# Performance work log

Measured on AMD Instinct MI355X. Metric: run time of the kernel, lower is better.

The kernel has to match this reference:

```python
import jax, jax.numpy as jnp
import numpy as np

B, T, L, H = 16, 16, 512, 768


def setup_inputs() -> dict:
    key = jax.random.key(0)
    k1, k2, k3, k4, k5, k6 = jax.random.split(key, 6)
    hn = jax.random.normal(k1, (B, L, H), dtype=jnp.float32)
    decoder_out = jax.random.normal(k2, (B, L, H), dtype=jnp.float32)
    W1 = jax.random.normal(k3, (H, H), dtype=jnp.float32) * (1.0 / np.sqrt(H))
    W2 = jax.random.normal(k4, (H, H), dtype=jnp.float32) * (1.0 / np.sqrt(H))
    V = jax.random.normal(k5, (H,), dtype=jnp.float32) * (1.0 / np.sqrt(H))
    # Ragged, consistent pointer indices: T monotone segment starts per sample,
    # gold boundary Yindex[b,t] in [Xindex[b,t], L).
    step = L // T  # 32
    Xindex = jnp.broadcast_to(jnp.arange(T, dtype=jnp.int64) * step, (B, T))
    offsets = jax.random.randint(k6, (B, T), 0, step, dtype=jnp.int64)
    Yindex = Xindex + offsets
    lens = jnp.full((B,), L, dtype=jnp.int64)
    return {"hn": hn, "decoder_out": decoder_out, "W1": W1, "W2": W2, "V": V,
            "Xindex": Xindex, "Yindex": Yindex, "lens": lens}


def reference(hn, decoder_out, W1, W2, V, Xindex, Yindex, lens):
    # Faithful batched form of training_decoder + pointerLayer:
    #   for each sample i, step j:
    #     en = hn[i, Xindex[i,j]:lens[i]]            (ragged suffix)
    #     dj = decoder_out[i, Yindex[i,j]]           (cur_dj = decoder_out[cur_groundy])
    #     s  = selu(V @ selu(W1 en + W2 dj))
    #     loss += NLL(log_softmax(s), Yindex[i,j]-Xindex[i,j])
    WE = jnp.einsum('blh,gh->blg', hn, W1)                        # [B,L,H]  nnW1(en)
    dj = jnp.take_along_axis(decoder_out, Yindex[:, :, None], axis=1)  # [B,T,H]
    WD = jnp.einsum('bth,gh->btg', dj, W2)                        # [B,T,H]  nnW2(dj)
    act = jax.nn.selu(WE[:, None, :, :] + WD[:, :, None, :])      # [B,T,L,H]
    scores = jax.nn.selu(jnp.einsum('btlh,h->btl', act, V))       # [B,T,L]
    pos = jnp.arange(hn.shape[1])
    mask = (pos[None, None, :] >= Xindex[:, :, None]) & (pos[None, None, :] < lens[:, None, None])
    neg_inf = jnp.finfo(scores.dtype).min
    masked = jnp.where(mask, scores, neg_inf)
    logp = masked - jax.scipy.special.logsumexp(masked, axis=-1, keepdims=True)
    # logits index (Yindex - Xindex) in the sliced array == global index Yindex
    gold = jnp.take_along_axis(logp, Yindex[:, :, None], axis=-1)[..., 0]  # [B,T]
    return -jnp.mean(gold)
```

## Files before the change

kernel.cpp:

```cpp
#include <hip/hip_runtime.h>
#include <hip/hip_bf16.h>
#include <math.h>

#define SELU_SCALE 1.0507009873554805f
#define SELU_ALPHA 1.6732632423543772f

static constexpr int B_ = 16, T_ = 16, L_ = 512, H_ = 768;

typedef __bf16 bf16x8 __attribute__((ext_vector_type(8)));
typedef float  f32x4  __attribute__((ext_vector_type(4)));

__device__ __forceinline__ float bf_lo(unsigned u) { return __uint_as_float(u << 16); }
__device__ __forceinline__ float bf_hi(unsigned u) { return __uint_as_float(u & 0xFFFF0000u); }

__device__ __forceinline__ float selu_core(float x) {
    float e = fmaf(__expf(x), SELU_ALPHA, -SELU_ALPHA);
    return x > 0.0f ? x : e;
}

__device__ __forceinline__ int xsw(int r) { return (r >> 1) & 3; }

__device__ __forceinline__ bf16x8 pack8(float4 a, float4 b) {
    bf16x8 o;
    o[0] = (__bf16)a.x; o[1] = (__bf16)a.y; o[2] = (__bf16)a.z; o[3] = (__bf16)a.w;
    o[4] = (__bf16)b.x; o[5] = (__bf16)b.y; o[6] = (__bf16)b.z; o[7] = (__bf16)b.w;
    return o;
}

__global__ __launch_bounds__(256, 2) void gemm_k(
        const float* __restrict__ hn, const float* __restrict__ dec,
        const float* __restrict__ w1, const float* __restrict__ w2,
        const int* __restrict__ Yi,
        __bf16* __restrict__ web, __bf16* __restrict__ wdb,
        float* __restrict__ out) {
    __shared__ __bf16 As[128 * 32];
    __shared__ __bf16 Bs[128 * 32];

    const int tid = threadIdx.x;
    if (blockIdx.x == 0 && tid == 0) out[0] = 0.0f;

    int bx = blockIdx.x;
    const float* Wf; __bf16* C; int m0, n0; bool wd;
    if (bx < 384) {
        wd = false; Wf = w1; C = web;
        m0 = (bx & 63) * 128; n0 = (bx >> 6) * 128;
    } else {
        wd = true; bx -= 384; Wf = w2; C = wdb;
        m0 = (bx & 1) * 128;  n0 = (bx >> 1) * 128;
    }

    const int wave = tid >> 6, lane = tid & 63;
    const int wm = (wave >> 1) * 64, wn = (wave & 1) * 64;
    const int lr = lane & 15, q = lane >> 4;

    const int r1 = wave * 32 + (lane >> 2);
    const int s3 = lane & 3;
    const int g1 = s3 ^ xsw(r1);

    const float *aG1, *aG2;
    if (!wd) {
        aG1 = hn + (size_t)(m0 + r1) * 768 + g1 * 8;
        aG2 = aG1 + (size_t)16 * 768;
    } else {
        int bt1 = m0 + r1, bt2 = bt1 + 16;
        aG1 = dec + ((size_t)((bt1 >> 4) * L_ + Yi[bt1])) * 768 + g1 * 8;
        aG2 = dec + ((size_t)((bt2 >> 4) * L_ + Yi[bt2])) * 768 + g1 * 8;
    }
    const float* bG1 = Wf + (size_t)(n0 + r1) * 768 + g1 * 8;
    const float* bG2 = bG1 + (size_t)16 * 768;

    bf16x8* AsW1 = (bf16x8*)&As[r1 * 32 + s3 * 8];
    bf16x8* AsW2 = (bf16x8*)&As[(r1 + 16) * 32 + s3 * 8];
    bf16x8* BsW1 = (bf16x8*)&Bs[r1 * 32 + s3 * 8];
    bf16x8* BsW2 = (bf16x8*)&Bs[(r1 + 16) * 32 + s3 * 8];

    int aoff[4], boff[4];
#pragma unroll
    for (int i = 0; i < 4; ++i) {
        int r = wm + i * 16 + lr;
        aoff[i] = r * 32 + (q ^ xsw(r)) * 8;
    }
#pragma unroll
    for (int j = 0; j < 4; ++j) {
        int r = wn + j * 16 + lr;
        boff[j] = r * 32 + (q ^ xsw(r)) * 8;
    }

    f32x4 acc[4][4] = {};

    float4 xa1a = *(const float4*)(aG1);      float4 xa1b = *(const float4*)(aG1 + 4);
    float4 xa2a = *(const float4*)(aG2);      float4 xa2b = *(const float4*)(aG2 + 4);
    float4 xb1a = *(const float4*)(bG1);      float4 xb1b = *(const float4*)(bG1 + 4);
    float4 xb2a = *(const float4*)(bG2);      float4 xb2b = *(const float4*)(bG2 + 4);
    float4 ya1a = *(const float4*)(aG1 + 32); float4 ya1b = *(const float4*)(aG1 + 36);
    float4 ya2a = *(const float4*)(aG2 + 32); float4 ya2b = *(const float4*)(aG2 + 36);
    float4 yb1a = *(const float4*)(bG1 + 32); float4 yb1b = *(const float4*)(bG1 + 36);
    float4 yb2a = *(const float4*)(bG2 + 32); float4 yb2b = *(const float4*)(bG2 + 36);

#pragma unroll 1
    for (int k0 = 0; k0 < 768; k0 += 64) {
        {
            *AsW1 = pack8(xa1a, xa1b);
            *AsW2 = pack8(xa2a, xa2b);
            *BsW1 = pack8(xb1a, xb1b);
            *BsW2 = pack8(xb2a, xb2b);
            asm volatile("s_waitcnt lgkmcnt(0)\n\ts_barrier" ::: "memory");
            if (k0 + 64 < 768) {
                xa1a = *(const float4*)(aG1 + k0 + 64); xa1b = *(const float4*)(aG1 + k0 + 68);
                xa2a = *(const float4*)(aG2 + k0 + 64); xa2b = *(const float4*)(aG2 + k0 + 68);
                xb1a = *(const float4*)(bG1 + k0 + 64); xb1b = *(const float4*)(bG1 + k0 + 68);
                xb2a = *(const float4*)(bG2 + k0 + 64); xb2b = *(const float4*)(bG2 + k0 + 68);
            }
            bf16x8 af[4], bfr[4];
#pragma unroll
            for (int i = 0; i < 4; ++i) af[i]  = *(const bf16x8*)&As[aoff[i]];
#pragma unroll
            for (int j = 0; j < 4; ++j) bfr[j] = *(const bf16x8*)&Bs[boff[j]];
#pragma unroll
            for (int i = 0; i < 4; ++i)
#pragma unroll
                for (int j = 0; j < 4; ++j)
                    acc[i][j] = __builtin_amdgcn_mfma_f32_16x16x32_bf16(af[i], bfr[j], acc[i][j], 0, 0, 0);
            asm volatile("s_barrier" ::: "memory");
        }
        {
            *AsW1 = pack8(ya1a, ya1b);
            *AsW2 = pack8(ya2a, ya2b);
            *BsW1 = pack8(yb1a, yb1b);
            *BsW2 = pack8(yb2a, yb2b);
            asm volatile("s_waitcnt lgkmcnt(0)\n\ts_barrier" ::: "memory");
            if (k0 + 96 < 768) {
                ya1a = *(const float4*)(aG1 + k0 + 96); ya1b = *(const float4*)(aG1 + k0 + 100);
                ya2a = *(const float4*)(aG2 + k0 + 96); ya2b = *(const float4*)(aG2 + k0 + 100);
                yb1a = *(const float4*)(bG1 + k0 + 96); yb1b = *(const float4*)(bG1 + k0 + 100);
                yb2a = *(const float4*)(bG2 + k0 + 96); yb2b = *(const float4*)(bG2 + k0 + 100);
            }
            bf16x8 af[4], bfr[4];
#pragma unroll
            for (int i = 0; i < 4; ++i) af[i]  = *(const bf16x8*)&As[aoff[i]];
#pragma unroll
            for (int j = 0; j < 4; ++j) bfr[j] = *(const bf16x8*)&Bs[boff[j]];
#pragma unroll
            for (int i = 0; i < 4; ++i)
#pragma unroll
                for (int j = 0; j < 4; ++j)
                    acc[i][j] = __builtin_amdgcn_mfma_f32_16x16x32_bf16(af[i], bfr[j], acc[i][j], 0, 0, 0);
            asm volatile("s_barrier" ::: "memory");
        }
    }

#pragma unroll
    for (int i = 0; i < 4; ++i)
#pragma unroll
        for (int j = 0; j < 4; ++j)
#pragma unroll
            for (int r = 0; r < 4; ++r) {
                int row = m0 + wm + i * 16 + q * 4 + r;
                int col = n0 + wn + j * 16 + lr;
                C[(size_t)row * 768 + col] = (__bf16)acc[i][j][r];
            }
}

__global__ __launch_bounds__(256) void scores_k(
        const __bf16* __restrict__ web, const __bf16* __restrict__ wdb,
        const float* __restrict__ V, const int* __restrict__ Xi,
        float* __restrict__ scores) {
    __shared__ float    we_s[16][772];
    __shared__ unsigned wd_s[16][388];
    __shared__ float    v_s[768];

    const int b = blockIdx.x, l0 = blockIdx.y * 16;

    for (int c = threadIdx.x; c < 16 * 96; c += 256) {
        int r = c / 96, cc = c % 96;
        uint4 v = *(const uint4*)(web + ((size_t)(b * L_ + l0 + r)) * H_ + cc * 8);
        float4 f0, f1;
        f0.x = bf_lo(v.x); f0.y = bf_hi(v.x); f0.z = bf_lo(v.y); f0.w = bf_hi(v.y);
        f1.x = bf_lo(v.z); f1.y = bf_hi(v.z); f1.z = bf_lo(v.w); f1.w = bf_hi(v.w);
        *(float4*)&we_s[r][cc * 8]     = f0;
        *(float4*)&we_s[r][cc * 8 + 4] = f1;
    }
    for (int c = threadIdx.x; c < 16 * 96; c += 256) {
        int r = c / 96, cc = c % 96;
        *(uint4*)&wd_s[r][cc * 4] = *(const uint4*)(wdb + ((size_t)(b * T_ + r)) * H_ + cc * 8);
    }
    if (threadIdx.x < 192) *(float4*)&v_s[threadIdx.x * 4] = ((const float4*)V)[threadIdx.x];
    __syncthreads();

    const int t = threadIdx.x >> 4;
    const int ls = threadIdx.x & 15;
    const int l = l0 + ls;
    const int X = Xi[b * T_ + t];
    if (!__any(l >= X)) return;

    float a0 = 0.f, a1 = 0.f, a2 = 0.f, a3 = 0.f;
#pragma unroll 4
    for (int h = 0; h < H_; h += 8) {
        float4 w0 = *(const float4*)&we_s[ls][h];
        float4 w1 = *(const float4*)&we_s[ls][h + 4];
        uint4  wd = *(const uint4*)&wd_s[t][h >> 1];
        float4 v0 = *(const float4*)&v_s[h];
        float4 v1 = *(const float4*)&v_s[h + 4];
        a0 = fmaf(selu_core(w0.x + bf_lo(wd.x)), v0.x, a0);
        a1 = fmaf(selu_core(w0.y + bf_hi(wd.x)), v0.y, a1);
        a2 = fmaf(selu_core(w0.z + bf_lo(wd.y)), v0.z, a2);
        a3 = fmaf(selu_core(w0.w + bf_hi(wd.y)), v0.w, a3);
        a0 = fmaf(selu_core(w1.x + bf_lo(wd.z)), v1.x, a0);
        a1 = fmaf(selu_core(w1.y + bf_hi(wd.z)), v1.y, a1);
        a2 = fmaf(selu_core(w1.z + bf_lo(wd.w)), v1.z, a2);
        a3 = fmaf(selu_core(w1.w + bf_hi(wd.w)), v1.w, a3);
    }
    float dot = SELU_SCALE * ((a0 + a1) + (a2 + a3));
    float sc  = dot > 0.0f ? SELU_SCALE * dot
                           : SELU_SCALE * SELU_ALPHA * (__expf(dot) - 1.0f);
    scores[((size_t)(b * T_ + t)) * L_ + l] = sc;
}

__global__ __launch_bounds__(64) void loss_k(
        const float* __restrict__ scores, const int* __restrict__ Xi,
        const int* __restrict__ Yi, float* __restrict__ out) {
    const int bt = blockIdx.x;
    const int lane = threadIdx.x;
    const int X = Xi[bt];
    const int Y = Yi[bt];
    const float* row = scores + (size_t)bt * L_;

    float m = -INFINITY;
    for (int l = X + lane; l < L_; l += 64) m = fmaxf(m, row[l]);
#pragma unroll
    for (int off = 32; off > 0; off >>= 1) m = fmaxf(m, __shfl_xor(m, off));

    float s = 0.0f;
    for (int l = X + lane; l < L_; l += 64) s += __expf(row[l] - m);
#pragma unroll
    for (int off = 32; off > 0; off >>= 1) s += __shfl_xor(s, off);

    if (lane == 0)
        atomicAdd(out, (m + __logf(s) - row[Y]) * (1.0f / (B_ * T_)));
}

extern "C" void kernel_launch(void* const* d_in, const int* in_sizes, int n_in,
                              void* d_out, int out_size, void* d_ws, size_t ws_size,
                              hipStream_t stream) {
    const float* hn  = (const float*)d_in[0];
    const float* dec = (const float*)d_in[1];
    const float* W1  = (const float*)d_in[2];
    const float* W2  = (const float*)d_in[3];
    const float* V   = (const float*)d_in[4];
    const int*   Xi  = (const int*)d_in[5];
    const int*   Yi  = (const int*)d_in[6];
    float* out = (float*)d_out;

    char* ws = (char*)d_ws;
    size_t off = 0;
    auto alloc = [&](size_t bytes) -> char* {
        char* p = ws + off;
        off += (bytes + 255) & ~(size_t)255;
        return p;
    };
    __bf16* web    = (__bf16*)alloc((size_t)B_ * L_ * H_ * 2);
    __bf16* wdb    = (__bf16*)alloc((size_t)B_ * T_ * H_ * 2);
    float*  scores = (float*)alloc((size_t)B_ * T_ * L_ * 4);

    gemm_k<<<396, 256, 0, stream>>>(hn, dec, W1, W2, Yi, web, wdb, out);
    scores_k<<<dim3(B_, L_ / 16), 256, 0, stream>>>(web, wdb, V, Xi, scores);
    loss_k<<<B_ * T_, 64, 0, stream>>>(scores, Xi, Yi, out);
}
```

Baseline: 155.9 us.

## Restructure scores kernel to register-resident WE rows with loop over T steps

The scores kernel now gives each thread 48 WE values and 48 V values held in registers, with 16 threads splitting the H dimension of one row l. It loops over the T decoder steps, reading WD directly from global memory, which is now stored as fp32, and combines the partial sums with a shuffle reduction. This drops the shared-memory staging and the per-thread full-H loop, and blocks are launched in reverse l order so the heavier tail blocks start first. The cost is higher register pressure, a serial loop over t per block, and twice the bytes for the WD buffer.

```diff
diff --git a/kernel.cpp b/kernel.cpp
--- a/kernel.cpp
+++ b/kernel.cpp
@@ -31,7 +31,7 @@
         const float* __restrict__ hn, const float* __restrict__ dec,
         const float* __restrict__ w1, const float* __restrict__ w2,
         const int* __restrict__ Yi,
-        __bf16* __restrict__ web, __bf16* __restrict__ wdb,
+        __bf16* __restrict__ web, float* __restrict__ wdf,
         float* __restrict__ out) {
     __shared__ __bf16 As[128 * 32];
     __shared__ __bf16 Bs[128 * 32];
@@ -40,12 +40,12 @@
     if (blockIdx.x == 0 && tid == 0) out[0] = 0.0f;
 
     int bx = blockIdx.x;
-    const float* Wf; __bf16* C; int m0, n0; bool wd;
+    const float* Wf; int m0, n0; bool wd;
     if (bx < 384) {
-        wd = false; Wf = w1; C = web;
+        wd = false; Wf = w1;
         m0 = (bx & 63) * 128; n0 = (bx >> 6) * 128;
     } else {
-        wd = true; bx -= 384; Wf = w2; C = wdb;
+        wd = true; bx -= 384; Wf = w2;
         m0 = (bx & 1) * 128;  n0 = (bx >> 1) * 128;
     }
 
@@ -157,63 +157,74 @@
             for (int r = 0; r < 4; ++r) {
                 int row = m0 + wm + i * 16 + q * 4 + r;
                 int col = n0 + wn + j * 16 + lr;
-                C[(size_t)row * 768 + col] = (__bf16)acc[i][j][r];
+                if (!wd) web[(size_t)row * 768 + col] = (__bf16)acc[i][j][r];
+                else     wdf[(size_t)row * 768 + col] = acc[i][j][r];
             }
 }
 
 __global__ __launch_bounds__(256) void scores_k(
-        const __bf16* __restrict__ web, const __bf16* __restrict__ wdb,
+        const __bf16* __restrict__ web, const float* __restrict__ wdf,
         const float* __restrict__ V, const int* __restrict__ Xi,
         float* __restrict__ scores) {
-    __shared__ float    we_s[16][772];
-    __shared__ unsigned wd_s[16][388];
-    __shared__ float    v_s[768];
-
-    const int b = blockIdx.x, l0 = blockIdx.y * 16;
-
-    for (int c = threadIdx.x; c < 16 * 96; c += 256) {
-        int r = c / 96, cc = c % 96;
-        uint4 v = *(const uint4*)(web + ((size_t)(b * L_ + l0 + r)) * H_ + cc * 8);
-        float4 f0, f1;
-        f0.x = bf_lo(v.x); f0.y = bf_hi(v.x); f0.z = bf_lo(v.y); f0.w = bf_hi(v.y);
-        f1.x = bf_lo(v.z); f1.y = bf_hi(v.z); f1.z = bf_lo(v.w); f1.w = bf_hi(v.w);
-        *(float4*)&we_s[r][cc * 8]     = f0;
-        *(float4*)&we_s[r][cc * 8 + 4] = f1;
-    }
-    for (int c = threadIdx.x; c < 16 * 96; c += 256) {
-        int r = c / 96, cc = c % 96;
-        *(uint4*)&wd_s[r][cc * 4] = *(const uint4*)(wdb + ((size_t)(b * T_ + r)) * H_ + cc * 8);
-    }
-    if (threadIdx.x < 192) *(float4*)&v_s[threadIdx.x * 4] = ((const float4*)V)[threadIdx.x];
-    __syncthreads();
-
-    const int t = threadIdx.x >> 4;
-    const int ls = threadIdx.x & 15;
-    const int l = l0 + ls;
-    const int X = Xi[b * T_ + t];
-    if (!__any(l >= X)) return;
-
-    float a0 = 0.f, a1 = 0.f, a2 = 0.f, a3 = 0.f;
-#pragma unroll 4
-    for (int h = 0; h < H_; h += 8) {
-        float4 w0 = *(const float4*)&we_s[ls][h];
-        float4 w1 = *(const float4*)&we_s[ls][h + 4];
-        uint4  wd = *(const uint4*)&wd_s[t][h >> 1];
-        float4 v0 = *(const float4*)&v_s[h];
-        float4 v1 = *(const float4*)&v_s[h + 4];
-        a0 = fmaf(selu_core(w0.x + bf_lo(wd.x)), v0.x, a0);
-        a1 = fmaf(selu_core(w0.y + bf_hi(wd.x)), v0.y, a1);
-        a2 = fmaf(selu_core(w0.z + bf_lo(wd.y)), v0.z, a2);
-        a3 = fmaf(selu_core(w0.w + bf_hi(wd.y)), v0.w, a3);
-        a0 = fmaf(selu_core(w1.x + bf_lo(wd.z)), v1.x, a0);
-        a1 = fmaf(selu_core(w1.y + bf_hi(wd.z)), v1.y, a1);
-        a2 = fmaf(selu_core(w1.z + bf_lo(wd.w)), v1.z, a2);
-        a3 = fmaf(selu_core(w1.w + bf_hi(wd.w)), v1.w, a3);
-    }
-    float dot = SELU_SCALE * ((a0 + a1) + (a2 + a3));
-    float sc  = dot > 0.0f ? SELU_SCALE * dot
-                           : SELU_SCALE * SELU_ALPHA * (__expf(dot) - 1.0f);
-    scores[((size_t)(b * T_ + t)) * L_ + l] = sc;
+    const int b  = blockIdx.x;
+    const int l0 = ((int)gridDim.y - 1 - (int)blockIdx.y) * 16;
+    const int tid = threadIdx.x;
+    const int ls = tid >> 4, hc = tid & 15;
+    const int l  = l0 + ls;
+    const int h0 = hc * 8;
+
+    float we[48], vv[48];
+    const __bf16* wr = web + ((size_t)(b * L_ + l)) * H_ + h0;
+#pragma unroll
+    for (int j = 0; j < 6; ++j) {
+        uint4 u = *(const uint4*)(wr + j * 128);
+        we[j*8+0] = bf_lo(u.x); we[j*8+1] = bf_hi(u.x);
+        we[j*8+2] = bf_lo(u.y); we[j*8+3] = bf_hi(u.y);
+        we[j*8+4] = bf_lo(u.z); we[j*8+5] = bf_hi(u.z);
+        we[j*8+6] = bf_lo(u.w); we[j*8+7] = bf_hi(u.w);
+    }
+    const float* vp = V + h0;
+#pragma unroll
+    for (int j = 0; j < 6; ++j) {
+        float4 a = *(const float4*)(vp + j * 128);
+        float4 c = *(const float4*)(vp + j * 128 + 4);
+        vv[j*8+0] = a.x; vv[j*8+1] = a.y; vv[j*8+2] = a.z; vv[j*8+3] = a.w;
+        vv[j*8+4] = c.x; vv[j*8+5] = c.y; vv[j*8+6] = c.z; vv[j*8+7] = c.w;
+    }
+
+    const int wmaxl = l0 + ((tid >> 6) << 2) + 3;
+    const int bT = b * T_;
+#pragma unroll 1
+    for (int t = 0; t < T_; ++t) {
+        const int X = Xi[bT + t];
+        if (wmaxl < X) continue;
+        const float* wdp = wdf + ((size_t)(bT + t)) * H_ + h0;
+        float a0 = 0.f, a1 = 0.f, a2 = 0.f, a3 = 0.f;
+#pragma unroll
+        for (int j = 0; j < 6; ++j) {
+            float4 x = *(const float4*)(wdp + j * 128);
+            float4 y = *(const float4*)(wdp + j * 128 + 4);
+            a0 = fmaf(selu_core(we[j*8+0] + x.x), vv[j*8+0], a0);
+            a1 = fmaf(selu_core(we[j*8+1] + x.y), vv[j*8+1], a1);
+            a2 = fmaf(selu_core(we[j*8+2] + x.z), vv[j*8+2], a2);
+            a3 = fmaf(selu_core(we[j*8+3] + x.w), vv[j*8+3], a3);
+            a0 = fmaf(selu_core(we[j*8+4] + y.x), vv[j*8+4], a0);
+            a1 = fmaf(selu_core(we[j*8+5] + y.y), vv[j*8+5], a1);
+            a2 = fmaf(selu_core(we[j*8+6] + y.z), vv[j*8+6], a2);
+            a3 = fmaf(selu_core(we[j*8+7] + y.w), vv[j*8+7], a3);
+        }
+        float dot = (a0 + a1) + (a2 + a3);
+        dot += __shfl_xor(dot, 1);
+        dot += __shfl_xor(dot, 2);
+        dot += __shfl_xor(dot, 4);
+        dot += __shfl_xor(dot, 8);
+        if (hc == 0) {
+            dot *= SELU_SCALE;
+            float sc = dot > 0.0f ? SELU_SCALE * dot
+                                  : SELU_SCALE * SELU_ALPHA * (__expf(dot) - 1.0f);
+            scores[((size_t)(bT + t)) * L_ + l] = sc;
+        }
+    }
 }
 
 __global__ __launch_bounds__(64) void loss_k(
@@ -259,10 +270,10 @@
         return p;
     };
     __bf16* web    = (__bf16*)alloc((size_t)B_ * L_ * H_ * 2);
-    __bf16* wdb    = (__bf16*)alloc((size_t)B_ * T_ * H_ * 2);
+    float*  wdf    = (float*)alloc((size_t)B_ * T_ * H_ * 4);
     float*  scores = (float*)alloc((size_t)B_ * T_ * L_ * 4);
 
-    gemm_k<<<396, 256, 0, stream>>>(hn, dec, W1, W2, Yi, web, wdb, out);
-    scores_k<<<dim3(B_, L_ / 16), 256, 0, stream>>>(web, wdb, V, Xi, scores);
+    gemm_k<<<396, 256, 0, stream>>>(hn, dec, W1, W2, Yi, web, wdf, out);
+    scores_k<<<dim3(B_, L_ / 16), 256, 0, stream>>>(web, wdf, V, Xi, scores);
     loss_k<<<B_ * T_, 64, 0, stream>>>(scores, Xi, Yi, out);
 }
```

After: 166.7 us. +6.9%, slower.
